# Kernel optimization log

Measured on AMD Instinct MI355X. Metric: run time of the kernel, lower is better.

## Reference

```python
import jax, jax.numpy as jnp
import numpy as np

VOCAB = 100000      # number of distinct seen item ids (len(table))
ID_SPACE = 120000   # total raw item-id space; ids >= VOCAB are 'unseen' -> -1


def setup_inputs() -> dict:
    key = jax.random.key(0)
    k1, k2, k3 = jax.random.split(key, 3)
    user_ids = jax.random.randint(k1, (16384,), 0, VOCAB, dtype=jnp.int64)
    item_ids = jax.random.randint(k2, (16384, 1000), 0, ID_SPACE, dtype=jnp.int64)
    # Lookup table emulating {item_id: frequency_rank}, with -1 for unseen ids.
    # Ranks are a permutation of [0, VOCAB) (sorted-by-count order), as floats
    # since the torch module writes them into a float tensor.
    ranks = jax.random.permutation(k3, VOCAB).astype(jnp.float32)
    lookup = jnp.concatenate(
        [ranks, jnp.full((ID_SPACE - VOCAB,), -1.0, dtype=jnp.float32)]
    )
    return {"user_ids": user_ids, "item_ids": item_ids, "lookup": lookup}


def reference(user_ids, item_ids, lookup):
    # scores[b, i] = table.get(item_ids[b, i], -1), vectorized as one gather.
    # user_ids is unused, matching the original forward.
    return lookup[item_ids]
```

## Files before the change

### kernel.cpp

```cpp
#include <hip/hip_runtime.h>
#include <hip/hip_bf16.h>


typedef unsigned int u32;

#define BLOCK   1024
#define QTOT    8
#define NSLICES 3
#define SLICE   40960
#define ROUNDS  10

__device__ __forceinline__ void gload_lds16(const float* g, float* l) {
    __builtin_amdgcn_global_load_lds(
        (const __attribute__((address_space(1))) u32*)g,
        (__attribute__((address_space(3))) u32*)l, 16, 0, 0);
}

__global__ void __launch_bounds__(BLOCK, 4)
FreqCounter_68315749810839_kernel(
    const int* __restrict__ ids,
    const float* __restrict__ lookup,
    float* __restrict__ out,
    long n4, int Tn)
{
    extern __shared__ float lds[];
    const int tid = threadIdx.x;
    const int wv  = tid >> 6;
    const int ln  = tid & 63;
    const int4* __restrict__ ids4 = (const int4*)ids;
    float4* __restrict__ out4 = (float4*)out;

    const long base = (long)blockIdx.x * (QTOT * BLOCK) + tid;

    int4 v[QTOT];
    float4 r[QTOT];
#pragma unroll
    for (int q = 0; q < QTOT; ++q) {
        long idx = base + (long)q * BLOCK;
        v[q] = (idx < n4) ? ids4[idx] : make_int4(0, 0, 0, 0);
        r[q] = make_float4(0.f, 0.f, 0.f, 0.f);
    }

    for (int s = 0; s < NSLICES; ++s) {
        const long lo = (long)s * SLICE;

        {
            float* lb = lds + wv * 256;
#pragma unroll
            for (int rr = 0; rr < ROUNDS; ++rr) {
                long gi = lo + rr * 4096 + wv * 256 + ln * 4;
                if (gi > (long)Tn - 4) gi = (long)Tn - 4;
                gload_lds16(lookup + gi, lb + rr * 4096);
            }
        }
        __syncthreads();

        const u32 lo2 = (u32)lo;
        const u32 remn = (u32)Tn - lo2;
        const u32 len = remn < (u32)SLICE ? remn : (u32)SLICE;

#define PR1(comp)                                                        \
        {                                                                \
            u32 d = (u32)v[q].comp - lo2;                                \
            u32 a = d < len ? d : 0u;       \
            float val = lds[a];                                          \
            if (d < len) r[q].comp = val;                                \
        }
#pragma unroll
        for (int q = 0; q < QTOT; ++q) {
            PR1(x) PR1(y) PR1(z) PR1(w)
        }
#undef PR1
        if (s + 1 < NSLICES) __syncthreads();
    }

#pragma unroll
    for (int q = 0; q < QTOT; ++q) {
        long idx = base + (long)q * BLOCK;
        if (idx < n4) out4[idx] = r[q];
    }
}

__global__ void FreqCounter_fallback_kernel(
    const int* __restrict__ ids, const float* __restrict__ lookup,
    float* __restrict__ out, long n)
{
    long i = (long)blockIdx.x * blockDim.x + threadIdx.x;
    const long stride = (long)gridDim.x * blockDim.x;
    for (; i < n; i += stride) out[i] = lookup[ids[i]];
}

__global__ void FreqCounter_tail_kernel(
    const int* __restrict__ ids, const float* __restrict__ lookup,
    float* __restrict__ out, long start, long n)
{
    long i = start + (long)blockIdx.x * blockDim.x + threadIdx.x;
    if (i < n) out[i] = lookup[ids[i]];
}

extern "C" void kernel_launch(void* const* d_in, const int* in_sizes, int n_in,
                              void* d_out, int out_size, void* d_ws, size_t ws_size,
                              hipStream_t stream) {
    const int*   ids    = (const int*)d_in[1];
    const float* lookup = (const float*)d_in[2];
    float*       out    = (float*)d_out;

    const long n  = (long)in_sizes[1];
    const int  Tn = in_sizes[2];

    if (Tn < 16 || Tn > NSLICES * SLICE || n < 4096) {
        long want = (n + 255) / 256;
        int grid = (int)(want < 2048 ? want : 2048);
        if (grid < 1) grid = 1;
        FreqCounter_fallback_kernel<<<grid, 256, 0, stream>>>(ids, lookup, out, n);
        return;
    }

    const long n4 = n / 4;
    const long qpb = (long)QTOT * BLOCK;
    const int grid = (int)((n4 + qpb - 1) / qpb);

    const size_t smem = (size_t)SLICE * sizeof(float);
    (void)hipFuncSetAttribute(
        reinterpret_cast<const void*>(FreqCounter_68315749810839_kernel),
        hipFuncAttributeMaxDynamicSharedMemorySize, (int)smem);

    FreqCounter_68315749810839_kernel<<<grid, BLOCK, smem, stream>>>(
        ids, lookup, out, n4, Tn);

    const long done = n4 * 4;
    if (done < n) {
        long rem = n - done;
        int tgrid = (int)((rem + 255) / 256);
        FreqCounter_tail_kernel<<<tgrid, 256, 0, stream>>>(ids, lookup, out, done, n);
    }
}
```

Baseline: 40.08 us.

## Prefetch next lookup slice into registers while gathering from current LDS slice

```diff
diff --git a/kernel.cpp b/kernel.cpp
--- a/kernel.cpp
+++ b/kernel.cpp
@@ -8,13 +8,7 @@
 #define QTOT    8
 #define NSLICES 3
 #define SLICE   40960
-#define ROUNDS  10
-
-__device__ __forceinline__ void gload_lds16(const float* g, float* l) {
-    __builtin_amdgcn_global_load_lds(
-        (const __attribute__((address_space(1))) u32*)g,
-        (__attribute__((address_space(3))) u32*)l, 16, 0, 0);
-}
+#define CH      10
 
 __global__ void __launch_bounds__(BLOCK, 4)
 FreqCounter_68315749810839_kernel(
@@ -24,13 +18,22 @@
     long n4, int Tn)
 {
     extern __shared__ float lds[];
+    float4* lds4 = (float4*)lds;
     const int tid = threadIdx.x;
-    const int wv  = tid >> 6;
-    const int ln  = tid & 63;
     const int4* __restrict__ ids4 = (const int4*)ids;
+    const float4* __restrict__ lk4 = (const float4*)lookup;
     float4* __restrict__ out4 = (float4*)out;
 
     const long base = (long)blockIdx.x * (QTOT * BLOCK) + tid;
+    const int total4 = Tn >> 2;
+
+    float4 st[CH];
+#pragma unroll
+    for (int c = 0; c < CH; ++c) {
+        int gi4 = c * BLOCK + tid;
+        if (gi4 > total4 - 1) gi4 = total4 - 1;
+        st[c] = lk4[gi4];
+    }
 
     int4 v[QTOT];
     float4 r[QTOT];
@@ -41,21 +44,22 @@
         r[q] = make_float4(0.f, 0.f, 0.f, 0.f);
     }
 
+#pragma unroll
+    for (int c = 0; c < CH; ++c) lds4[c * BLOCK + tid] = st[c];
+    __syncthreads();
+
     for (int s = 0; s < NSLICES; ++s) {
-        const long lo = (long)s * SLICE;
-
-        {
-            float* lb = lds + wv * 256;
+        if (s + 1 < NSLICES) {
+            const int nb4 = (s + 1) * (SLICE >> 2);
 #pragma unroll
-            for (int rr = 0; rr < ROUNDS; ++rr) {
-                long gi = lo + rr * 4096 + wv * 256 + ln * 4;
-                if (gi > (long)Tn - 4) gi = (long)Tn - 4;
-                gload_lds16(lookup + gi, lb + rr * 4096);
+            for (int c = 0; c < CH; ++c) {
+                int gi4 = nb4 + c * BLOCK + tid;
+                if (gi4 > total4 - 1) gi4 = total4 - 1;
+                st[c] = lk4[gi4];
             }
         }
-        __syncthreads();
 
-        const u32 lo2 = (u32)lo;
+        const u32 lo2 = (u32)(s * SLICE);
         const u32 remn = (u32)Tn - lo2;
         const u32 len = remn < (u32)SLICE ? remn : (u32)SLICE;
 
@@ -71,7 +75,13 @@
             PR1(x) PR1(y) PR1(z) PR1(w)
         }
 #undef PR1
-        if (s + 1 < NSLICES) __syncthreads();
+        __syncthreads();
+
+        if (s + 1 < NSLICES) {
+#pragma unroll
+            for (int c = 0; c < CH; ++c) lds4[c * BLOCK + tid] = st[c];
+            __syncthreads();
+        }
     }
 
 #pragma unroll
@@ -108,7 +118,7 @@
     const long n  = (long)in_sizes[1];
     const int  Tn = in_sizes[2];
 
-    if (Tn < 16 || Tn > NSLICES * SLICE || n < 4096) {
+    if (Tn < 16 || (Tn & 3) || Tn > NSLICES * SLICE || n < 4096) {
         long want = (n + 255) / 256;
         int grid = (int)(want < 2048 ? want : 2048);
         if (grid < 1) grid = 1;
```

After: 103.8 us. 2.59x slower.
